# Kernel tuning notes

Hardware: AMD Instinct MI355X
Metric: run time of the kernel (lower is better)

The kernel has to match this reference:

```python
import jax, jax.numpy as jnp
import numpy as np

D_K = 64  # key/query head dim used for the 1/sqrt(d_k) scale


def setup_inputs() -> dict:
    key0 = jax.random.key(0)
    kk, kq, kv = jax.random.split(key0, 3)
    B, H, S, DK, DV = 2, 16, 2048, 64, 64
    return {
        "key": jax.random.normal(kk, (B, H, S, DK), dtype=jnp.float32),
        "query": jax.random.normal(kq, (B, H, S, DK), dtype=jnp.float32),
        "value": jax.random.normal(kv, (B, H, S, DV), dtype=jnp.float32),
    }


def reference(key, query, value):
    # scaled dot-product attention per head: [B,H,S,S]
    scores = jnp.einsum("bhqd,bhkd->bhqk", query, key) / jnp.sqrt(jnp.asarray(D_K, query.dtype))
    attn = jax.nn.softmax(scores, axis=-1)
    out = jnp.einsum("bhqk,bhkv->bhqv", attn, value)  # [B,H,S,d_v]
    B, H, S, DV = out.shape
    # faithful to the torch .view: raw reshape (no head transpose)
    return out.reshape(B, S, H * DV)
```

## Files before the change

kernel.cpp:

```cpp
#include <hip/hip_runtime.h>

#define S_LEN 2048
#define DHEAD 64
#define BHEADS 32
#define NTILES 32
#define HEAD_ELEMS (S_LEN * DHEAD)
#define TENS_ELEMS (BHEADS * HEAD_ELEMS)
#define TILE_HALVES 4096

typedef _Float16 half8_t __attribute__((ext_vector_type(8)));
typedef _Float16 half4_t __attribute__((ext_vector_type(4)));
typedef _Float16 half2_t __attribute__((ext_vector_type(2)));
typedef float float4_t __attribute__((ext_vector_type(4)));

#define SC_LOG2E 0.18033688011112042f


__global__ __launch_bounds__(256) void prep_kernel(const float* __restrict__ K,
                                                   const float* __restrict__ V,
                                                   _Float16* __restrict__ Kf,
                                                   _Float16* __restrict__ Vf) {
    __shared__ _Float16 tile[64][72];
    const int bh = blockIdx.x >> 5;
    const int t = blockIdx.x & 31;
    const int tid = threadIdx.x;

    const float* Ksrc = K + (bh * S_LEN + t * 64) * DHEAD;
    const float4* vs = (const float4*)(V + (bh * S_LEN + t * 64) * DHEAD);
#pragma unroll
    for (int it = 0; it < 4; ++it) {
        int i = it * 256 + tid;
        float4 vv = vs[i];
        int r = i >> 4, c4 = (i & 15) * 4;
        half4_t hv = {(_Float16)vv.x, (_Float16)vv.y, (_Float16)vv.z, (_Float16)vv.w};
        *(half4_t*)&tile[r][c4] = hv;
    }

    _Float16* kd = Kf + (bh * NTILES + t) * TILE_HALVES;
#pragma unroll
    for (int it = 0; it < 2; ++it) {
        int c = it * 256 + tid;
        int f = c >> 6, lane = c & 63;
        int row = (f >> 1) * 16 + (lane & 15);
        int d0 = (f & 1) * 32 + (lane >> 4) * 8;
        const float4* s = (const float4*)(Ksrc + row * DHEAD + d0);
        float4 a = s[0], b = s[1];
        half8_t h = {(_Float16)(a.x * SC_LOG2E), (_Float16)(a.y * SC_LOG2E),
                     (_Float16)(a.z * SC_LOG2E), (_Float16)(a.w * SC_LOG2E),
                     (_Float16)(b.x * SC_LOG2E), (_Float16)(b.y * SC_LOG2E),
                     (_Float16)(b.z * SC_LOG2E), (_Float16)(b.w * SC_LOG2E)};
        *(half8_t*)(kd + c * 8) = h;
    }
    __syncthreads();

    _Float16* vd = Vf + (bh * NTILES + t) * TILE_HALVES;
#pragma unroll
    for (int it = 0; it < 2; ++it) {
        int c = it * 256 + tid;
        int fv = c >> 6, lane = c & 63;
        int vt = fv >> 1, ktp = fv & 1;
        int v = vt * 16 + (lane & 15);
        int g = lane >> 4;
        half8_t h;
#pragma unroll
        for (int j = 0; j < 8; ++j) {
            int key = ktp * 32 + (j >> 2) * 16 + g * 4 + (j & 3);
            h[j] = tile[key][v];
        }
        *(half8_t*)(vd + c * 8) = h;
    }
}


__global__ __launch_bounds__(256, 2) void attn_kernel(
    const float* __restrict__ Qf,
    const _Float16* __restrict__ Kf,
    const _Float16* __restrict__ Vf,
    float* __restrict__ out) {
    const int tid = threadIdx.x;
    const int wid = tid >> 6;
    const int lane = tid & 63;
    const int ln15 = lane & 15;
    const int g = lane >> 4;

    const int gwave = blockIdx.x * 4 + wid;
    const int bh = gwave >> 6;
    const int q0 = (gwave & 63) * 32;

    const float* Qg = Qf + (bh * S_LEN + q0) * DHEAD;
    half8_t qf[2][2];
#pragma unroll
    for (int nq = 0; nq < 2; ++nq)
#pragma unroll
        for (int kh = 0; kh < 2; ++kh) {
            const float4* qs = (const float4*)(Qg + (nq * 16 + ln15) * DHEAD + kh * 32 + g * 8);
            float4 a = qs[0], b = qs[1];
            qf[nq][kh] = (half8_t){(_Float16)a.x, (_Float16)a.y, (_Float16)a.z, (_Float16)a.w,
                                   (_Float16)b.x, (_Float16)b.y, (_Float16)b.z, (_Float16)b.w};
        }

    const _Float16* kb = Kf + bh * (NTILES * TILE_HALVES);
    const _Float16* vb = Vf + bh * (NTILES * TILE_HALVES);
    const int lo = lane * 8;

    half8_t kf[2][8], vf[2][8];
#pragma unroll
    for (int f = 0; f < 8; ++f) {
        kf[0][f] = *(const half8_t*)(kb + f * 512 + lo);
        vf[0][f] = *(const half8_t*)(vb + f * 512 + lo);
    }

    float lsum[2] = {0.f, 0.f};
    float4_t o[2][4];
#pragma unroll
    for (int nq = 0; nq < 2; ++nq)
#pragma unroll
        for (int vt = 0; vt < 4; ++vt) o[nq][vt] = (float4_t){0.f, 0.f, 0.f, 0.f};

#pragma unroll 2
    for (int t = 0; t < NTILES; ++t) {
        const int cur = t & 1;
        const int tn = (t + 1 < NTILES) ? t + 1 : t;
        const _Float16* kbn = kb + tn * TILE_HALVES;
        const _Float16* vbn = vb + tn * TILE_HALVES;
#pragma unroll
        for (int f = 0; f < 8; ++f) {
            kf[cur ^ 1][f] = *(const half8_t*)(kbn + f * 512 + lo);
            vf[cur ^ 1][f] = *(const half8_t*)(vbn + f * 512 + lo);
        }

        half4_t pb[2][4];
#pragma unroll
        for (int mt = 0; mt < 4; ++mt) {
            half8_t a0 = kf[cur][mt * 2];
            half8_t a1 = kf[cur][mt * 2 + 1];
#pragma unroll
            for (int nq = 0; nq < 2; ++nq) {
                float4_t c0 = (float4_t){0.f, 0.f, 0.f, 0.f};
                c0 = __builtin_amdgcn_mfma_f32_16x16x32_f16(a0, qf[nq][0], c0, 0, 0, 0);
                c0 = __builtin_amdgcn_mfma_f32_16x16x32_f16(a1, qf[nq][1], c0, 0, 0, 0);
                float p0 = __builtin_amdgcn_exp2f(c0[0]);
                float p1 = __builtin_amdgcn_exp2f(c0[1]);
                float p2 = __builtin_amdgcn_exp2f(c0[2]);
                float p3 = __builtin_amdgcn_exp2f(c0[3]);
                lsum[nq] += (p0 + p1) + (p2 + p3);
                half2_t plo = __builtin_bit_cast(half2_t, __builtin_amdgcn_cvt_pkrtz(p0, p1));
                half2_t phi = __builtin_bit_cast(half2_t, __builtin_amdgcn_cvt_pkrtz(p2, p3));
                pb[nq][mt] = (half4_t){plo[0], plo[1], phi[0], phi[1]};
            }
        }

#pragma unroll
        for (int vt = 0; vt < 4; ++vt) {
#pragma unroll
            for (int ktp = 0; ktp < 2; ++ktp) {
                half8_t va = vf[cur][vt * 2 + ktp];
                half4_t alo = __builtin_shufflevector(va, va, 0, 1, 2, 3);
                half4_t ahi = __builtin_shufflevector(va, va, 4, 5, 6, 7);
#pragma unroll
                for (int nq = 0; nq < 2; ++nq) {
                    o[nq][vt] = __builtin_amdgcn_mfma_f32_16x16x16f16(alo, pb[nq][2 * ktp], o[nq][vt], 0, 0, 0);
                    o[nq][vt] = __builtin_amdgcn_mfma_f32_16x16x16f16(ahi, pb[nq][2 * ktp + 1], o[nq][vt], 0, 0, 0);
                }
            }
        }
    }

#pragma unroll
    for (int nq = 0; nq < 2; ++nq) {
        float l = lsum[nq];
        l += __shfl_xor(l, 16, 64);
        l += __shfl_xor(l, 32, 64);
        float inv_l = 1.0f / l;
        int qg = q0 + nq * 16 + ln15;
        float* og = out + (bh * S_LEN + qg) * DHEAD;
#pragma unroll
        for (int vt = 0; vt < 4; ++vt) {
            float4_t vals;
            vals[0] = o[nq][vt][0] * inv_l;
            vals[1] = o[nq][vt][1] * inv_l;
            vals[2] = o[nq][vt][2] * inv_l;
            vals[3] = o[nq][vt][3] * inv_l;
            *(float4_t*)(og + vt * 16 + g * 4) = vals;
        }
    }
}


extern "C" void kernel_launch(void* const* d_in, const int* in_sizes, int n_in,
                              void* d_out, int out_size, void* d_ws, size_t ws_size,
                              hipStream_t stream) {
    const float* Kin = (const float*)d_in[0];
    const float* Qin = (const float*)d_in[1];
    const float* Vin = (const float*)d_in[2];
    float* out = (float*)d_out;

    _Float16* Kf = (_Float16*)d_ws;
    _Float16* Vf = Kf + TENS_ELEMS;

    prep_kernel<<<BHEADS * NTILES, 256, 0, stream>>>(Kin, Vin, Kf, Vf);
    attn_kernel<<<BHEADS * 64 / 4, 256, 0, stream>>>(Qin, Kf, Vf, out);
}
```

Measured before the change: 137.8 us.

## Split key range across wave pairs and reduce partial attention in shared memory

Each block now handles 64 queries with two query groups, and each group's KV sequence is split in half across two waves. The partial outputs and row sums are combined through shared memory before normalisation. The grid doubles from 512 to 1024 blocks, and launch bounds rise to 4 blocks per CU, to raise wave count and occupancy on the many-CU GPU. The cost is an LDS reduction, a block barrier and tighter register limits. The softmax skips max subtraction, so summing the split partials is still exact.

```diff
diff --git a/kernel.cpp b/kernel.cpp
--- a/kernel.cpp
+++ b/kernel.cpp
@@ -72,20 +72,25 @@
 }
 
 
-__global__ __launch_bounds__(256, 2) void attn_kernel(
+__global__ __launch_bounds__(256, 4) void attn_kernel(
     const float* __restrict__ Qf,
     const _Float16* __restrict__ Kf,
     const _Float16* __restrict__ Vf,
     float* __restrict__ out) {
+    __shared__ float red[2][34][64];
+
     const int tid = threadIdx.x;
     const int wid = tid >> 6;
     const int lane = tid & 63;
     const int ln15 = lane & 15;
     const int g = lane >> 4;
 
-    const int gwave = blockIdx.x * 4 + wid;
-    const int bh = gwave >> 6;
-    const int q0 = (gwave & 63) * 32;
+    const int bh = blockIdx.x >> 5;
+    const int qpair = blockIdx.x & 31;
+    const int qg = wid >> 1;
+    const int ks = wid & 1;
+    const int q0 = qpair * 64 + qg * 32;
+    const int t0 = ks * 16;
 
     const float* Qg = Qf + (bh * S_LEN + q0) * DHEAD;
     half8_t qf[2][2];
@@ -99,8 +104,8 @@
                                    (_Float16)b.x, (_Float16)b.y, (_Float16)b.z, (_Float16)b.w};
         }
 
-    const _Float16* kb = Kf + bh * (NTILES * TILE_HALVES);
-    const _Float16* vb = Vf + bh * (NTILES * TILE_HALVES);
+    const _Float16* kb = Kf + bh * (NTILES * TILE_HALVES) + t0 * TILE_HALVES;
+    const _Float16* vb = Vf + bh * (NTILES * TILE_HALVES) + t0 * TILE_HALVES;
     const int lo = lane * 8;
 
     half8_t kf[2][8], vf[2][8];
@@ -118,9 +123,9 @@
         for (int vt = 0; vt < 4; ++vt) o[nq][vt] = (float4_t){0.f, 0.f, 0.f, 0.f};
 
 #pragma unroll 2
-    for (int t = 0; t < NTILES; ++t) {
+    for (int t = 0; t < 16; ++t) {
         const int cur = t & 1;
-        const int tn = (t + 1 < NTILES) ? t + 1 : t;
+        const int tn = (t + 1 < 16) ? t + 1 : t;
         const _Float16* kbn = kb + tn * TILE_HALVES;
         const _Float16* vbn = vb + tn * TILE_HALVES;
 #pragma unroll
@@ -171,17 +176,36 @@
         float l = lsum[nq];
         l += __shfl_xor(l, 16, 64);
         l += __shfl_xor(l, 32, 64);
-        float inv_l = 1.0f / l;
-        int qg = q0 + nq * 16 + ln15;
-        float* og = out + (bh * S_LEN + qg) * DHEAD;
-#pragma unroll
-        for (int vt = 0; vt < 4; ++vt) {
-            float4_t vals;
-            vals[0] = o[nq][vt][0] * inv_l;
-            vals[1] = o[nq][vt][1] * inv_l;
-            vals[2] = o[nq][vt][2] * inv_l;
-            vals[3] = o[nq][vt][3] * inv_l;
-            *(float4_t*)(og + vt * 16 + g * 4) = vals;
+        lsum[nq] = l;
+    }
+
+    if (ks == 1) {
+#pragma unroll
+        for (int nq = 0; nq < 2; ++nq)
+#pragma unroll
+            for (int vt = 0; vt < 4; ++vt)
+#pragma unroll
+                for (int r = 0; r < 4; ++r)
+                    red[qg][nq * 16 + vt * 4 + r][lane] = o[nq][vt][r];
+        red[qg][32][lane] = lsum[0];
+        red[qg][33][lane] = lsum[1];
+    }
+    __syncthreads();
+    if (ks == 0) {
+#pragma unroll
+        for (int nq = 0; nq < 2; ++nq) {
+            float lt = lsum[nq] + red[qg][32 + nq][lane];
+            float inv_l = 1.0f / lt;
+            int qg_global = q0 + nq * 16 + ln15;
+            float* og = out + (bh * S_LEN + qg_global) * DHEAD;
+#pragma unroll
+            for (int vt = 0; vt < 4; ++vt) {
+                float4_t vals;
+#pragma unroll
+                for (int r = 0; r < 4; ++r)
+                    vals[r] = (o[nq][vt][r] + red[qg][nq * 16 + vt * 4 + r][lane]) * inv_l;
+                *(float4_t*)(og + vt * 16 + g * 4) = vals;
+            }
         }
     }
 }
@@ -199,5 +223,5 @@
     _Float16* Vf = Kf + TENS_ELEMS;
 
     prep_kernel<<<BHEADS * NTILES, 256, 0, stream>>>(Kin, Vin, Kf, Vf);
-    attn_kernel<<<BHEADS * 64 / 4, 256, 0, stream>>>(Qin, Kf, Vf, out);
+    attn_kernel<<<BHEADS * 32, 256, 0, stream>>>(Qin, Kf, Vf, out);
 }
```

New measurement: 168.7 us. +22.5%, slower.
